# Optimization experiments

Measured on AMD Instinct MI355X. Metric: run time of the kernel, lower is better.

## Reference

```python
import jax, jax.numpy as jnp
import numpy as np

NEG_SLOPE = 0.2  # PyG GATConv default


def setup_inputs() -> dict:
    key = jax.random.key(0)
    k1, k2, k3, k4, k5, k6 = jax.random.split(key, 6)
    N, F_in, F_out, E = 50000, 512, 256, 400000
    x = jax.random.normal(k1, (N, F_in), dtype=jnp.float32)
    adj = jax.random.randint(k2, (2, E), 0, N, dtype=jnp.int64)  # [2, E] edge_index (src, dst)
    glorot = lambda k, shape: jax.random.uniform(
        k, shape, jnp.float32, -1.0, 1.0) * np.sqrt(6.0 / (shape[0] + shape[-1]))
    W = glorot(k3, (F_in, F_out))
    att_src = glorot(k4, (F_out,))
    att_dst = glorot(k5, (F_out,))
    bias = jnp.zeros((F_out,), dtype=jnp.float32)
    return {"x": x, "adj": adj, "W": W, "att_src": att_src, "att_dst": att_dst, "bias": bias}


def reference(x, adj, W, att_src, att_dst, bias):
    N = x.shape[0]
    # add self loops (PyG GATConv default add_self_loops=True)
    loops = jnp.arange(N, dtype=adj.dtype)
    src = jnp.concatenate([adj[0], loops])
    dst = jnp.concatenate([adj[1], loops])

    h = x @ W                          # [N, F_out] projected features
    a_src = h @ att_src                # [N] per-node source attention term
    a_dst = h @ att_dst                # [N]
    e = a_src[src] + a_dst[dst]        # [E+N] edge logits
    e = jnp.where(e > 0, e, NEG_SLOPE * e)  # leaky_relu

    # per-destination softmax over incoming edges (numerically stable)
    m = jax.ops.segment_max(e, dst, num_segments=N)
    ex = jnp.exp(e - m[dst])
    denom = jax.ops.segment_sum(ex, dst, num_segments=N)
    alpha = ex / denom[dst]            # [E+N]

    # weighted scatter-aggregate of source messages
    out = jax.ops.segment_sum(alpha[:, None] * h[src], dst, num_segments=N)
    out = out + bias
    return jax.nn.relu(out)
```

## Files before the change

kernel.cpp:

```cpp
#include <hip/hip_runtime.h>
#include <hip/hip_bf16.h>

typedef __attribute__((ext_vector_type(8))) short bf16x8;
typedef __attribute__((ext_vector_type(4))) float f32x4;
typedef unsigned short u16;

#define F_IN 512
#define F_OUT 256
#define NEG_SLOPE 0.2f

__device__ __forceinline__ float leaky(float e) { return e > 0.f ? e : NEG_SLOPE * e; }

__device__ __forceinline__ u16 f2bf(float x) {
    __hip_bfloat16 h = __float2bfloat16(x);
    return *reinterpret_cast<u16*>(&h);
}
__device__ __forceinline__ void bf2x2(unsigned p, float& a, float& b) {
    a = __uint_as_float(p << 16);
    b = __uint_as_float(p & 0xffff0000u);
}

__device__ __forceinline__ void dma16(const void* g, void* l) {
    __builtin_amdgcn_global_load_lds((const __attribute__((address_space(1))) void*)g,
                                     (__attribute__((address_space(3))) void*)l, 16, 0, 0);
}

__global__ void k_transpose(const float* __restrict__ W, u16* __restrict__ Wt,
                            int* __restrict__ deg, int N) {
    int t = blockIdx.x * 256 + threadIdx.x;
    int k = t >> 8;
    int n = t & 255;
    Wt[n * F_IN + k] = f2bf(W[k * F_OUT + n]);
    if (t < N) deg[t] = 0;
}

__global__ __launch_bounds__(256) void k_gemm(const float* __restrict__ X,
                                              const u16* __restrict__ Wt,
                                              const float* __restrict__ att_src,
                                              const float* __restrict__ att_dst,
                                              u16* __restrict__ Hb,
                                              float* __restrict__ aS, float* __restrict__ aD,
                                              int N) {
    __shared__ float sA[4][64 * 32];
    const int tid = threadIdx.x;
    const int wave = tid >> 6, lane = tid & 63;
    const int tile_m = blockIdx.x * 64;
    const int lm = lane & 15, q = lane >> 4;

    const int a_row_in = lane >> 3;
    const int a_gc = (lane & 7) ^ a_row_in;
    const float* aG[2];
#pragma unroll
    for (int t = 0; t < 2; ++t) {
        int grow = tile_m + wave * 16 + t * 8 + a_row_in;
        if (grow >= N) grow = N - 1;
        aG[t] = &X[(size_t)grow * F_IN + a_gc * 4];
    }
    const u16* bP[4];
#pragma unroll
    for (int j = 0; j < 4; j++)
        bP[j] = &Wt[(size_t)(wave * 64 + j * 16 + lm) * F_IN + q * 8];

    f32x4 acc[4][4];
#pragma unroll
    for (int i = 0; i < 4; i++)
#pragma unroll
        for (int j = 0; j < 4; j++) acc[i][j] = (f32x4){0.f, 0.f, 0.f, 0.f};

    auto dmaA = [&](int kb) {
        const int buf = kb & 3;
#pragma unroll
        for (int t = 0; t < 2; ++t)
            dma16(aG[t] + kb * 32, &sA[buf][(wave * 16 + t * 8) * 32]);
    };
    dmaA(0);
    dmaA(1);

    for (int kb = 0; kb < F_IN / 32; ++kb) {
        bf16x8 bfr[4];
#pragma unroll
        for (int j = 0; j < 4; j++) bfr[j] = *(const bf16x8*)(bP[j] + kb * 32);
        if (kb + 2 < F_IN / 32) dmaA(kb + 2);
        asm volatile("s_waitcnt vmcnt(4)" ::: "memory");
        __builtin_amdgcn_sched_barrier(0);
        __builtin_amdgcn_s_barrier();

        const int buf = kb & 3;
        bf16x8 af[4];
#pragma unroll
        for (int i = 0; i < 4; i++) {
            const int arow = i * 16 + lm;
            const int s7 = arow & 7;
            const float4 c0 = *(const float4*)&sA[buf][arow * 32 + (((2 * q) ^ s7) << 2)];
            const float4 c1 = *(const float4*)&sA[buf][arow * 32 + (((2 * q + 1) ^ s7) << 2)];
            u16 a8[8] = {f2bf(c0.x), f2bf(c0.y), f2bf(c0.z), f2bf(c0.w),
                         f2bf(c1.x), f2bf(c1.y), f2bf(c1.z), f2bf(c1.w)};
            af[i] = *(const bf16x8*)a8;
        }
#pragma unroll
        for (int i = 0; i < 4; i++)
#pragma unroll
            for (int j = 0; j < 4; j++)
                acc[i][j] = __builtin_amdgcn_mfma_f32_16x16x32_bf16(af[i], bfr[j], acc[i][j], 0, 0, 0);
    }
    __syncthreads();

    float vS[4], vD[4];
#pragma unroll
    for (int j = 0; j < 4; ++j) {
        int col = wave * 64 + j * 16 + lm;
        vS[j] = att_src[col];
        vD[j] = att_dst[col];
    }
    float* sD = (float*)sA;
#pragma unroll
    for (int i = 0; i < 4; i++) {
#pragma unroll
        for (int r = 0; r < 4; r++) {
            float pS = acc[i][0][r] * vS[0] + acc[i][1][r] * vS[1] +
                       acc[i][2][r] * vS[2] + acc[i][3][r] * vS[3];
            float pD = acc[i][0][r] * vD[0] + acc[i][1][r] * vD[1] +
                       acc[i][2][r] * vD[2] + acc[i][3][r] * vD[3];
#pragma unroll
            for (int off = 1; off < 16; off <<= 1) {
                pS += __shfl_xor(pS, off);
                pD += __shfl_xor(pD, off);
            }
            if (lm == 0) {
                int rl = i * 16 + q * 4 + r;
                sD[rl * 8 + wave * 2 + 0] = pS;
                sD[rl * 8 + wave * 2 + 1] = pD;
            }
        }
    }
    __syncthreads();
    if (tid < 64) {
        int row = tile_m + tid;
        if (row < N) {
            aS[row] = sD[tid * 8 + 0] + sD[tid * 8 + 2] + sD[tid * 8 + 4] + sD[tid * 8 + 6];
            aD[row] = sD[tid * 8 + 1] + sD[tid * 8 + 3] + sD[tid * 8 + 5] + sD[tid * 8 + 7];
        }
    }

#pragma unroll
    for (int i = 0; i < 4; i++)
#pragma unroll
        for (int j = 0; j < 4; j++) {
#pragma unroll
            for (int r = 0; r < 4; r++) {
                int row = tile_m + i * 16 + q * 4 + r;
                int col = wave * 64 + j * 16 + lm;
                if (row < N) Hb[(size_t)row * F_OUT + col] = f2bf(acc[i][j][r]);
            }
        }
}

__global__ void k_deg(const int* __restrict__ dsts, int* __restrict__ deg, int E) {
    int e = blockIdx.x * 256 + threadIdx.x;
    if (e >= E) return;
    atomicAdd(&deg[dsts[e]], 1);
}

__global__ __launch_bounds__(256) void k_scan1(const int* __restrict__ deg,
                                               int* __restrict__ bsum, int N) {
    __shared__ int ws[4];
    int t = threadIdx.x;
    int i = blockIdx.x * 256 + t;
    int v = (i < N) ? deg[i] : 0;
    for (int off = 32; off; off >>= 1) v += __shfl_down(v, off);
    if ((t & 63) == 0) ws[t >> 6] = v;
    __syncthreads();
    if (t == 0) bsum[blockIdx.x] = ws[0] + ws[1] + ws[2] + ws[3];
}

__global__ __launch_bounds__(256) void k_scan2(const int* __restrict__ bsum,
                                               int* __restrict__ boff, int* __restrict__ offs,
                                               int nb, int N) {
    __shared__ int ss[256];
    int t = threadIdx.x;
    int v = (t < nb) ? bsum[t] : 0;
    ss[t] = v;
    __syncthreads();
    for (int off = 1; off < 256; off <<= 1) {
        int u = (t >= off) ? ss[t - off] : 0;
        __syncthreads();
        ss[t] += u;
        __syncthreads();
    }
    boff[t] = ss[t] - v;
    if (t == 255) offs[N] = ss[255];
}

__global__ __launch_bounds__(256) void k_scan3(const int* __restrict__ deg,
                                               const int* __restrict__ boff,
                                               int* __restrict__ offs, int* __restrict__ cur,
                                               int N) {
    __shared__ int ss[256];
    int t = threadIdx.x;
    int i = blockIdx.x * 256 + t;
    int v = (i < N) ? deg[i] : 0;
    ss[t] = v;
    __syncthreads();
    for (int off = 1; off < 256; off <<= 1) {
        int u = (t >= off) ? ss[t - off] : 0;
        __syncthreads();
        ss[t] += u;
        __syncthreads();
    }
    int ex = ss[t] - v + boff[blockIdx.x];
    if (i < N) {
        offs[i] = ex;
        cur[i] = ex;
    }
}

__global__ void k_edge_scatter(const int* __restrict__ srcs, const int* __restrict__ dsts,
                               const float* __restrict__ aS, const float* __restrict__ aD,
                               int* __restrict__ cur, int* __restrict__ csrS,
                               float* __restrict__ csrW, int E) {
    int e = blockIdx.x * 256 + threadIdx.x;
    if (e >= E) return;
    int s = srcs[e], d = dsts[e];
    float ex = __expf(leaky(aS[s] + aD[d]));
    int pos = atomicAdd(&cur[d], 1);
    csrS[pos] = s;
    csrW[pos] = ex;
}

__global__ __launch_bounds__(256) void k_aggregate(const u16* __restrict__ Hb,
                                                   const float* __restrict__ aS,
                                                   const float* __restrict__ aD,
                                                   const int* __restrict__ offs,
                                                   const int* __restrict__ csrS,
                                                   const float* __restrict__ csrW,
                                                   const float* __restrict__ bias,
                                                   float* __restrict__ out, int N) {
    int wave = threadIdx.x >> 6, lane = threadIdx.x & 63;
    int i = blockIdx.x * 4 + wave;
    if (i >= N) return;
    float sex = __expf(leaky(aS[i] + aD[i]));

    uint2 rv = *(const uint2*)&Hb[(size_t)i * F_OUT + lane * 4];
    float f0, f1, f2, f3;
    bf2x2(rv.x, f0, f1);
    bf2x2(rv.y, f2, f3);
    float4 acc = {sex * f0, sex * f1, sex * f2, sex * f3};
    float wsum = sex;

    int beg = offs[i], end = offs[i + 1];
    int k = beg;
    for (; k + 4 <= end; k += 4) {
        int s0 = csrS[k], s1 = csrS[k + 1], s2 = csrS[k + 2], s3 = csrS[k + 3];
        float w0 = csrW[k], w1 = csrW[k + 1], w2 = csrW[k + 2], w3 = csrW[k + 3];
        uint2 g0 = *(const uint2*)&Hb[(size_t)s0 * F_OUT + lane * 4];
        uint2 g1 = *(const uint2*)&Hb[(size_t)s1 * F_OUT + lane * 4];
        uint2 g2 = *(const uint2*)&Hb[(size_t)s2 * F_OUT + lane * 4];
        uint2 g3 = *(const uint2*)&Hb[(size_t)s3 * F_OUT + lane * 4];
        wsum += w0 + w1 + w2 + w3;
        bf2x2(g0.x, f0, f1); bf2x2(g0.y, f2, f3);
        acc.x += w0 * f0; acc.y += w0 * f1; acc.z += w0 * f2; acc.w += w0 * f3;
        bf2x2(g1.x, f0, f1); bf2x2(g1.y, f2, f3);
        acc.x += w1 * f0; acc.y += w1 * f1; acc.z += w1 * f2; acc.w += w1 * f3;
        bf2x2(g2.x, f0, f1); bf2x2(g2.y, f2, f3);
        acc.x += w2 * f0; acc.y += w2 * f1; acc.z += w2 * f2; acc.w += w2 * f3;
        bf2x2(g3.x, f0, f1); bf2x2(g3.y, f2, f3);
        acc.x += w3 * f0; acc.y += w3 * f1; acc.z += w3 * f2; acc.w += w3 * f3;
    }
    for (; k < end; ++k) {
        int s = csrS[k];
        float w = csrW[k];
        uint2 r = *(const uint2*)&Hb[(size_t)s * F_OUT + lane * 4];
        wsum += w;
        bf2x2(r.x, f0, f1);
        bf2x2(r.y, f2, f3);
        acc.x += w * f0;
        acc.y += w * f1;
        acc.z += w * f2;
        acc.w += w * f3;
    }
    float inv = 1.f / wsum;
    const float4 bv = *(const float4*)&bias[lane * 4];
    float4 o;
    o.x = acc.x * inv + bv.x;
    o.y = acc.y * inv + bv.y;
    o.z = acc.z * inv + bv.z;
    o.w = acc.w * inv + bv.w;
    o.x = o.x > 0.f ? o.x : 0.f;
    o.y = o.y > 0.f ? o.y : 0.f;
    o.z = o.z > 0.f ? o.z : 0.f;
    o.w = o.w > 0.f ? o.w : 0.f;
    *(float4*)&out[(size_t)i * F_OUT + lane * 4] = o;
}

extern "C" void kernel_launch(void* const* d_in, const int* in_sizes, int n_in,
                              void* d_out, int out_size, void* d_ws, size_t ws_size,
                              hipStream_t stream) {
    const float* X = (const float*)d_in[0];
    const int* adj = (const int*)d_in[1];
    const float* W = (const float*)d_in[2];
    const float* att_src = (const float*)d_in[3];
    const float* att_dst = (const float*)d_in[4];
    const float* bias = (const float*)d_in[5];
    float* out = (float*)d_out;

    const int N = in_sizes[0] / F_IN;
    const int E = in_sizes[1] / 2;
    const int* srcs = adj;
    const int* dsts = adj + E;
    const int nb = (N + 255) / 256;

    char* p = (char*)d_ws;
    auto take = [&](size_t b) -> char* {
        char* q = p;
        p += (b + 255) & ~(size_t)255;
        return q;
    };
    u16* Hb = (u16*)take((size_t)N * F_OUT * sizeof(u16));
    u16* Wt = (u16*)take((size_t)F_IN * F_OUT * sizeof(u16));
    float* aS = (float*)take((size_t)N * sizeof(float));
    float* aD = (float*)take((size_t)N * sizeof(float));
    int* deg = (int*)take((size_t)N * sizeof(int));
    int* offs = (int*)take((size_t)(N + 1) * sizeof(int));
    int* cur = (int*)take((size_t)N * sizeof(int));
    int* bsum = (int*)take((size_t)256 * sizeof(int));
    int* boff = (int*)take((size_t)256 * sizeof(int));
    int* csrS = (int*)take((size_t)E * sizeof(int));
    float* csrW = (float*)take((size_t)E * sizeof(float));

    k_transpose<<<(F_IN * F_OUT) / 256, 256, 0, stream>>>(W, Wt, deg, N);
    k_gemm<<<(N + 63) / 64, 256, 0, stream>>>(X, Wt, att_src, att_dst, Hb, aS, aD, N);
    k_deg<<<(E + 255) / 256, 256, 0, stream>>>(dsts, deg, E);
    k_scan1<<<nb, 256, 0, stream>>>(deg, bsum, N);
    k_scan2<<<1, 256, 0, stream>>>(bsum, boff, offs, nb, N);
    k_scan3<<<nb, 256, 0, stream>>>(deg, boff, offs, cur, N);
    k_edge_scatter<<<(E + 255) / 256, 256, 0, stream>>>(srcs, dsts, aS, aD, cur, csrS, csrW, E);
    k_aggregate<<<(N + 3) / 4, 256, 0, stream>>>(Hb, aS, aD, offs, csrS, csrW, bias, out, N);
}
```

Baseline: 291.6 us.

## Load GEMM A operand directly into registers with a 2x2 wave tiling

The projection GEMM no longer stages X tiles through LDS with global_load_lds DMA and barriers. Each wave now loads its A fragments straight from global memory into registers, prefetching one k-step ahead, and the waves are arranged as a 2x2 grid of 32 rows by 128 columns. Dropping the big shared buffer and the per-step barriers, together with launch bounds of 3 blocks, is meant to raise occupancy and remove sync overhead. In exchange each wave loads more B (W) data per step, and the X reads become strided 32-byte loads per row with no LDS reuse across waves.

```diff
diff --git a/kernel.cpp b/kernel.cpp
--- a/kernel.cpp
+++ b/kernel.cpp
@@ -18,11 +18,6 @@
 __device__ __forceinline__ void bf2x2(unsigned p, float& a, float& b) {
     a = __uint_as_float(p << 16);
     b = __uint_as_float(p & 0xffff0000u);
-}
-
-__device__ __forceinline__ void dma16(const void* g, void* l) {
-    __builtin_amdgcn_global_load_lds((const __attribute__((address_space(1))) void*)g,
-                                     (__attribute__((address_space(3))) void*)l, 16, 0, 0);
 }
 
 __global__ void k_transpose(const float* __restrict__ W, u16* __restrict__ Wt,
@@ -34,102 +29,97 @@
     if (t < N) deg[t] = 0;
 }
 
-__global__ __launch_bounds__(256) void k_gemm(const float* __restrict__ X,
-                                              const u16* __restrict__ Wt,
-                                              const float* __restrict__ att_src,
-                                              const float* __restrict__ att_dst,
-                                              u16* __restrict__ Hb,
-                                              float* __restrict__ aS, float* __restrict__ aD,
-                                              int N) {
-    __shared__ float sA[4][64 * 32];
+__global__ __launch_bounds__(256, 3) void k_gemm(const float* __restrict__ X,
+                                                 const u16* __restrict__ Wt,
+                                                 const float* __restrict__ att_src,
+                                                 const float* __restrict__ att_dst,
+                                                 u16* __restrict__ Hb,
+                                                 float* __restrict__ aS, float* __restrict__ aD,
+                                                 int N) {
+    __shared__ float sD[64 * 4];
     const int tid = threadIdx.x;
     const int wave = tid >> 6, lane = tid & 63;
+    const int wr = wave >> 1, wc = wave & 1;
     const int tile_m = blockIdx.x * 64;
     const int lm = lane & 15, q = lane >> 4;
 
-    const int a_row_in = lane >> 3;
-    const int a_gc = (lane & 7) ^ a_row_in;
-    const float* aG[2];
-#pragma unroll
-    for (int t = 0; t < 2; ++t) {
-        int grow = tile_m + wave * 16 + t * 8 + a_row_in;
-        if (grow >= N) grow = N - 1;
-        aG[t] = &X[(size_t)grow * F_IN + a_gc * 4];
-    }
-    const u16* bP[4];
-#pragma unroll
-    for (int j = 0; j < 4; j++)
-        bP[j] = &Wt[(size_t)(wave * 64 + j * 16 + lm) * F_IN + q * 8];
-
-    f32x4 acc[4][4];
-#pragma unroll
-    for (int i = 0; i < 4; i++)
-#pragma unroll
-        for (int j = 0; j < 4; j++) acc[i][j] = (f32x4){0.f, 0.f, 0.f, 0.f};
-
-    auto dmaA = [&](int kb) {
-        const int buf = kb & 3;
-#pragma unroll
-        for (int t = 0; t < 2; ++t)
-            dma16(aG[t] + kb * 32, &sA[buf][(wave * 16 + t * 8) * 32]);
-    };
-    dmaA(0);
-    dmaA(1);
-
-    for (int kb = 0; kb < F_IN / 32; ++kb) {
-        bf16x8 bfr[4];
-#pragma unroll
-        for (int j = 0; j < 4; j++) bfr[j] = *(const bf16x8*)(bP[j] + kb * 32);
-        if (kb + 2 < F_IN / 32) dmaA(kb + 2);
-        asm volatile("s_waitcnt vmcnt(4)" ::: "memory");
-        __builtin_amdgcn_sched_barrier(0);
-        __builtin_amdgcn_s_barrier();
-
-        const int buf = kb & 3;
-        bf16x8 af[4];
-#pragma unroll
-        for (int i = 0; i < 4; i++) {
-            const int arow = i * 16 + lm;
-            const int s7 = arow & 7;
-            const float4 c0 = *(const float4*)&sA[buf][arow * 32 + (((2 * q) ^ s7) << 2)];
-            const float4 c1 = *(const float4*)&sA[buf][arow * 32 + (((2 * q + 1) ^ s7) << 2)];
-            u16 a8[8] = {f2bf(c0.x), f2bf(c0.y), f2bf(c0.z), f2bf(c0.w),
-                         f2bf(c1.x), f2bf(c1.y), f2bf(c1.z), f2bf(c1.w)};
-            af[i] = *(const bf16x8*)a8;
-        }
-#pragma unroll
-        for (int i = 0; i < 4; i++)
-#pragma unroll
-            for (int j = 0; j < 4; j++)
-                acc[i][j] = __builtin_amdgcn_mfma_f32_16x16x32_bf16(af[i], bfr[j], acc[i][j], 0, 0, 0);
-    }
-    __syncthreads();
-
-    float vS[4], vD[4];
-#pragma unroll
-    for (int j = 0; j < 4; ++j) {
-        int col = wave * 64 + j * 16 + lm;
+    const float* aP0;
+    const float* aP1;
+    {
+        int r0 = tile_m + wr * 32 + 0 * 16 + lm;
+        int r1 = tile_m + wr * 32 + 1 * 16 + lm;
+        if (r0 >= N) r0 = N - 1;
+        if (r1 >= N) r1 = N - 1;
+        aP0 = &X[(size_t)r0 * F_IN + q * 8];
+        aP1 = &X[(size_t)r1 * F_IN + q * 8];
+    }
+    const u16* bBase = &Wt[(size_t)(wc * 128 + lm) * F_IN + q * 8];
+
+    f32x4 acc[2][8];
+#pragma unroll
+    for (int i = 0; i < 2; i++)
+#pragma unroll
+        for (int j = 0; j < 8; j++) acc[i][j] = (f32x4){0.f, 0.f, 0.f, 0.f};
+
+    float4 c00 = *(const float4*)(aP0);
+    float4 c01 = *(const float4*)(aP0 + 4);
+    float4 c10 = *(const float4*)(aP1);
+    float4 c11 = *(const float4*)(aP1 + 4);
+
+#pragma unroll
+    for (int ks = 0; ks < F_IN / 32; ++ks) {
+        const int o = ks * 32;
+        bf16x8 bf[8];
+#pragma unroll
+        for (int j = 0; j < 8; j++)
+            bf[j] = *(const bf16x8*)(bBase + (size_t)j * 16 * F_IN + o);
+        float4 n00, n01, n10, n11;
+        if (ks + 1 < F_IN / 32) {
+            n00 = *(const float4*)(aP0 + o + 32);
+            n01 = *(const float4*)(aP0 + o + 36);
+            n10 = *(const float4*)(aP1 + o + 32);
+            n11 = *(const float4*)(aP1 + o + 36);
+        }
+        u16 a0[8] = {f2bf(c00.x), f2bf(c00.y), f2bf(c00.z), f2bf(c00.w),
+                     f2bf(c01.x), f2bf(c01.y), f2bf(c01.z), f2bf(c01.w)};
+        u16 a1[8] = {f2bf(c10.x), f2bf(c10.y), f2bf(c10.z), f2bf(c10.w),
+                     f2bf(c11.x), f2bf(c11.y), f2bf(c11.z), f2bf(c11.w)};
+        bf16x8 af0 = *(const bf16x8*)a0;
+        bf16x8 af1 = *(const bf16x8*)a1;
+#pragma unroll
+        for (int j = 0; j < 8; j++) {
+            acc[0][j] = __builtin_amdgcn_mfma_f32_16x16x32_bf16(af0, bf[j], acc[0][j], 0, 0, 0);
+            acc[1][j] = __builtin_amdgcn_mfma_f32_16x16x32_bf16(af1, bf[j], acc[1][j], 0, 0, 0);
+        }
+        c00 = n00; c01 = n01; c10 = n10; c11 = n11;
+    }
+
+    float vS[8], vD[8];
+#pragma unroll
+    for (int j = 0; j < 8; ++j) {
+        int col = wc * 128 + j * 16 + lm;
         vS[j] = att_src[col];
         vD[j] = att_dst[col];
     }
-    float* sD = (float*)sA;
-#pragma unroll
-    for (int i = 0; i < 4; i++) {
+#pragma unroll
+    for (int i = 0; i < 2; i++) {
 #pragma unroll
         for (int r = 0; r < 4; r++) {
-            float pS = acc[i][0][r] * vS[0] + acc[i][1][r] * vS[1] +
-                       acc[i][2][r] * vS[2] + acc[i][3][r] * vS[3];
-            float pD = acc[i][0][r] * vD[0] + acc[i][1][r] * vD[1] +
-                       acc[i][2][r] * vD[2] + acc[i][3][r] * vD[3];
+            float pS = 0.f, pD = 0.f;
+#pragma unroll
+            for (int j = 0; j < 8; j++) {
+                pS += acc[i][j][r] * vS[j];
+                pD += acc[i][j][r] * vD[j];
+            }
 #pragma unroll
             for (int off = 1; off < 16; off <<= 1) {
                 pS += __shfl_xor(pS, off);
                 pD += __shfl_xor(pD, off);
             }
             if (lm == 0) {
-                int rl = i * 16 + q * 4 + r;
-                sD[rl * 8 + wave * 2 + 0] = pS;
-                sD[rl * 8 + wave * 2 + 1] = pD;
+                int rl = wr * 32 + i * 16 + q * 4 + r;
+                sD[rl * 4 + wc * 2 + 0] = pS;
+                sD[rl * 4 + wc * 2 + 1] = pD;
             }
         }
     }
@@ -137,19 +127,19 @@
     if (tid < 64) {
         int row = tile_m + tid;
         if (row < N) {
-            aS[row] = sD[tid * 8 + 0] + sD[tid * 8 + 2] + sD[tid * 8 + 4] + sD[tid * 8 + 6];
-            aD[row] = sD[tid * 8 + 1] + sD[tid * 8 + 3] + sD[tid * 8 + 5] + sD[tid * 8 + 7];
-        }
-    }
-
-#pragma unroll
-    for (int i = 0; i < 4; i++)
-#pragma unroll
-        for (int j = 0; j < 4; j++) {
+            aS[row] = sD[tid * 4 + 0] + sD[tid * 4 + 2];
+            aD[row] = sD[tid * 4 + 1] + sD[tid * 4 + 3];
+        }
+    }
+
+#pragma unroll
+    for (int i = 0; i < 2; i++)
+#pragma unroll
+        for (int j = 0; j < 8; j++) {
 #pragma unroll
             for (int r = 0; r < 4; r++) {
-                int row = tile_m + i * 16 + q * 4 + r;
-                int col = wave * 64 + j * 16 + lm;
+                int row = tile_m + wr * 32 + i * 16 + q * 4 + r;
+                int col = wc * 128 + j * 16 + lm;
                 if (row < N) Hb[(size_t)row * F_OUT + col] = f2bf(acc[i][j][r]);
             }
         }
```

After: 338.4 us. +16.0%, slower.

## Stage W tiles in LDS for GEMM and pack CSR source/weight pairs

Applied to the files above, without the earlier changes.

The GEMM now loads W tiles through global-to-LDS DMA into a swizzled shared buffer instead of reading them from global into registers. It drops the 4-deep A prefetch ring for a single buffer with two barriers per k-step, which gives up overlap of loads with MFMA. The CSR source index and edge weight are packed into one int2 array so the scatter and aggregate kernels do one access per edge instead of two. The aggregate loop is unrolled to 8 edges so more gathers are in flight at once.

```diff
diff --git a/kernel.cpp b/kernel.cpp
--- a/kernel.cpp
+++ b/kernel.cpp
@@ -41,7 +41,8 @@
                                               u16* __restrict__ Hb,
                                               float* __restrict__ aS, float* __restrict__ aD,
                                               int N) {
-    __shared__ float sA[4][64 * 32];
+    __shared__ float sA[64 * 32];
+    __shared__ u16 sB[256 * 32];
     const int tid = threadIdx.x;
     const int wave = tid >> 6, lane = tid & 63;
     const int tile_m = blockIdx.x * 64;
@@ -56,10 +57,14 @@
         if (grow >= N) grow = N - 1;
         aG[t] = &X[(size_t)grow * F_IN + a_gc * 4];
     }
-    const u16* bP[4];
-#pragma unroll
-    for (int j = 0; j < 4; j++)
-        bP[j] = &Wt[(size_t)(wave * 64 + j * 16 + lm) * F_IN + q * 8];
+    const int b_col_in = lane >> 2;
+    const int b_gc = (lane & 3) ^ (b_col_in & 3);
+    const u16* bG[4];
+#pragma unroll
+    for (int t = 0; t < 4; ++t) {
+        int col = wave * 64 + t * 16 + b_col_in;
+        bG[t] = &Wt[(size_t)col * F_IN + b_gc * 8];
+    }
 
     f32x4 acc[4][4];
 #pragma unroll
@@ -67,43 +72,38 @@
 #pragma unroll
         for (int j = 0; j < 4; j++) acc[i][j] = (f32x4){0.f, 0.f, 0.f, 0.f};
 
-    auto dmaA = [&](int kb) {
-        const int buf = kb & 3;
+    for (int kb = 0; kb < F_IN / 32; ++kb) {
 #pragma unroll
         for (int t = 0; t < 2; ++t)
-            dma16(aG[t] + kb * 32, &sA[buf][(wave * 16 + t * 8) * 32]);
-    };
-    dmaA(0);
-    dmaA(1);
-
-    for (int kb = 0; kb < F_IN / 32; ++kb) {
-        bf16x8 bfr[4];
-#pragma unroll
-        for (int j = 0; j < 4; j++) bfr[j] = *(const bf16x8*)(bP[j] + kb * 32);
-        if (kb + 2 < F_IN / 32) dmaA(kb + 2);
-        asm volatile("s_waitcnt vmcnt(4)" ::: "memory");
-        __builtin_amdgcn_sched_barrier(0);
-        __builtin_amdgcn_s_barrier();
-
-        const int buf = kb & 3;
-        bf16x8 af[4];
+            dma16(aG[t] + kb * 32, &sA[(wave * 16 + t * 8) * 32]);
+#pragma unroll
+        for (int t = 0; t < 4; ++t)
+            dma16(bG[t] + kb * 32, &sB[(wave * 64 + t * 16) * 32]);
+        __syncthreads();
+
+        bf16x8 af[4], bfr[4];
 #pragma unroll
         for (int i = 0; i < 4; i++) {
             const int arow = i * 16 + lm;
-            const int s7 = arow & 7;
-            const float4 c0 = *(const float4*)&sA[buf][arow * 32 + (((2 * q) ^ s7) << 2)];
-            const float4 c1 = *(const float4*)&sA[buf][arow * 32 + (((2 * q + 1) ^ s7) << 2)];
+            const int s7 = lm & 7;
+            const float4 c0 = *(const float4*)&sA[arow * 32 + (((2 * q) ^ s7) << 2)];
+            const float4 c1 = *(const float4*)&sA[arow * 32 + (((2 * q + 1) ^ s7) << 2)];
             u16 a8[8] = {f2bf(c0.x), f2bf(c0.y), f2bf(c0.z), f2bf(c0.w),
                          f2bf(c1.x), f2bf(c1.y), f2bf(c1.z), f2bf(c1.w)};
             af[i] = *(const bf16x8*)a8;
         }
 #pragma unroll
+        for (int j = 0; j < 4; j++) {
+            const int col = wave * 64 + j * 16 + lm;
+            bfr[j] = *(const bf16x8*)&sB[col * 32 + ((q ^ (lm & 3)) << 3)];
+        }
+#pragma unroll
         for (int i = 0; i < 4; i++)
 #pragma unroll
             for (int j = 0; j < 4; j++)
                 acc[i][j] = __builtin_amdgcn_mfma_f32_16x16x32_bf16(af[i], bfr[j], acc[i][j], 0, 0, 0);
-    }
-    __syncthreads();
+        __syncthreads();
+    }
 
     float vS[4], vD[4];
 #pragma unroll
@@ -216,23 +216,20 @@
 
 __global__ void k_edge_scatter(const int* __restrict__ srcs, const int* __restrict__ dsts,
                                const float* __restrict__ aS, const float* __restrict__ aD,
-                               int* __restrict__ cur, int* __restrict__ csrS,
-                               float* __restrict__ csrW, int E) {
+                               int* __restrict__ cur, int2* __restrict__ csrP, int E) {
     int e = blockIdx.x * 256 + threadIdx.x;
     if (e >= E) return;
     int s = srcs[e], d = dsts[e];
     float ex = __expf(leaky(aS[s] + aD[d]));
     int pos = atomicAdd(&cur[d], 1);
-    csrS[pos] = s;
-    csrW[pos] = ex;
+    csrP[pos] = make_int2(s, __float_as_int(ex));
 }
 
 __global__ __launch_bounds__(256) void k_aggregate(const u16* __restrict__ Hb,
                                                    const float* __restrict__ aS,
                                                    const float* __restrict__ aD,
                                                    const int* __restrict__ offs,
-                                                   const int* __restrict__ csrS,
-                                                   const float* __restrict__ csrW,
+                                                   const int2* __restrict__ csrP,
                                                    const float* __restrict__ bias,
                                                    float* __restrict__ out, int N) {
     int wave = threadIdx.x >> 6, lane = threadIdx.x & 63;
@@ -249,27 +246,45 @@
 
     int beg = offs[i], end = offs[i + 1];
     int k = beg;
-    for (; k + 4 <= end; k += 4) {
-        int s0 = csrS[k], s1 = csrS[k + 1], s2 = csrS[k + 2], s3 = csrS[k + 3];
-        float w0 = csrW[k], w1 = csrW[k + 1], w2 = csrW[k + 2], w3 = csrW[k + 3];
-        uint2 g0 = *(const uint2*)&Hb[(size_t)s0 * F_OUT + lane * 4];
-        uint2 g1 = *(const uint2*)&Hb[(size_t)s1 * F_OUT + lane * 4];
-        uint2 g2 = *(const uint2*)&Hb[(size_t)s2 * F_OUT + lane * 4];
-        uint2 g3 = *(const uint2*)&Hb[(size_t)s3 * F_OUT + lane * 4];
-        wsum += w0 + w1 + w2 + w3;
-        bf2x2(g0.x, f0, f1); bf2x2(g0.y, f2, f3);
-        acc.x += w0 * f0; acc.y += w0 * f1; acc.z += w0 * f2; acc.w += w0 * f3;
-        bf2x2(g1.x, f0, f1); bf2x2(g1.y, f2, f3);
-        acc.x += w1 * f0; acc.y += w1 * f1; acc.z += w1 * f2; acc.w += w1 * f3;
-        bf2x2(g2.x, f0, f1); bf2x2(g2.y, f2, f3);
-        acc.x += w2 * f0; acc.y += w2 * f1; acc.z += w2 * f2; acc.w += w2 * f3;
-        bf2x2(g3.x, f0, f1); bf2x2(g3.y, f2, f3);
-        acc.x += w3 * f0; acc.y += w3 * f1; acc.z += w3 * f2; acc.w += w3 * f3;
+    for (; k + 8 <= end; k += 8) {
+        int2 pp[8];
+        uint2 gg[8];
+#pragma unroll
+        for (int u = 0; u < 8; ++u) pp[u] = csrP[k + u];
+#pragma unroll
+        for (int u = 0; u < 8; ++u)
+            gg[u] = *(const uint2*)&Hb[(size_t)pp[u].x * F_OUT + lane * 4];
+#pragma unroll
+        for (int u = 0; u < 8; ++u) {
+            float w = __int_as_float(pp[u].y);
+            wsum += w;
+            bf2x2(gg[u].x, f0, f1);
+            bf2x2(gg[u].y, f2, f3);
+            acc.x += w * f0; acc.y += w * f1; acc.z += w * f2; acc.w += w * f3;
+        }
+    }
+    if (k + 4 <= end) {
+        int2 pp[4];
+        uint2 gg[4];
+#pragma unroll
+        for (int u = 0; u < 4; ++u) pp[u] = csrP[k + u];
+#pragma unroll
+        for (int u = 0; u < 4; ++u)
+            gg[u] = *(const uint2*)&Hb[(size_t)pp[u].x * F_OUT + lane * 4];
+#pragma unroll
+        for (int u = 0; u < 4; ++u) {
+            float w = __int_as_float(pp[u].y);
+            wsum += w;
+            bf2x2(gg[u].x, f0, f1);
+            bf2x2(gg[u].y, f2, f3);
+            acc.x += w * f0; acc.y += w * f1; acc.z += w * f2; acc.w += w * f3;
+        }
+        k += 4;
     }
     for (; k < end; ++k) {
-        int s = csrS[k];
-        float w = csrW[k];
-        uint2 r = *(const uint2*)&Hb[(size_t)s * F_OUT + lane * 4];
+        int2 p = csrP[k];
+        float w = __int_as_float(p.y);
+        uint2 r = *(const uint2*)&Hb[(size_t)p.x * F_OUT + lane * 4];
         wsum += w;
         bf2x2(r.x, f0, f1);
         bf2x2(r.y, f2, f3);
@@ -324,8 +339,7 @@
     int* cur = (int*)take((size_t)N * sizeof(int));
     int* bsum = (int*)take((size_t)256 * sizeof(int));
     int* boff = (int*)take((size_t)256 * sizeof(int));
-    int* csrS = (int*)take((size_t)E * sizeof(int));
-    float* csrW = (float*)take((size_t)E * sizeof(float));
+    int2* csrP = (int2*)take((size_t)E * sizeof(int2));
 
     k_transpose<<<(F_IN * F_OUT) / 256, 256, 0, stream>>>(W, Wt, deg, N);
     k_gemm<<<(N + 63) / 64, 256, 0, stream>>>(X, Wt, att_src, att_dst, Hb, aS, aD, N);
@@ -333,6 +347,6 @@
     k_scan1<<<nb, 256, 0, stream>>>(deg, bsum, N);
     k_scan2<<<1, 256, 0, stream>>>(bsum, boff, offs, nb, N);
     k_scan3<<<nb, 256, 0, stream>>>(deg, boff, offs, cur, N);
-    k_edge_scatter<<<(E + 255) / 256, 256, 0, stream>>>(srcs, dsts, aS, aD, cur, csrS, csrW, E);
-    k_aggregate<<<(N + 3) / 4, 256, 0, stream>>>(Hb, aS, aD, offs, csrS, csrW, bias, out, N);
-}
+    k_edge_scatter<<<(E + 255) / 256, 256, 0, stream>>>(srcs, dsts, aS, aD, cur, csrP, E);
+    k_aggregate<<<(N + 3) / 4, 256, 0, stream>>>(Hb, aS, aD, offs, csrP, bias, out, N);
+}
```

Measured after the change: 283.6 us. -2.8%, faster.
